# Optimization experiments

Measured on AMD Instinct MI355X. Metric: run time of the kernel, lower is better.

## Reference

```python
import jax, jax.numpy as jnp
import numpy as np

B, T, D, E, I = 8, 8192, 128, 8, 16
EPS = 1e-5


def setup_inputs() -> dict:
    key = jax.random.key(0)
    ks = jax.random.split(key, 6)
    return {
        "x": jax.random.normal(ks[0], (B, T, D), dtype=jnp.float32),
        "ln_g": jnp.ones((D,), dtype=jnp.float32),
        "ln_b": jnp.zeros((D,), dtype=jnp.float32),
        "gate_w": jax.random.normal(ks[1], (D, E), dtype=jnp.float32) * (1.0 / np.sqrt(D)),
        "gate_b": jnp.zeros((E,), dtype=jnp.float32),
        "w1": jax.random.normal(ks[2], (E, D, I), dtype=jnp.float32),
        "w2": jax.random.normal(ks[3], (E, I, D), dtype=jnp.float32),
    }


def reference(x, ln_g, ln_b, gate_w, gate_b, w1, w2):
    # LayerNorm (torch default eps=1e-5)
    mu = jnp.mean(x, axis=-1, keepdims=True)
    var = jnp.mean(jnp.square(x - mu), axis=-1, keepdims=True)
    x_norm = (x - mu) * jax.lax.rsqrt(var + EPS) * ln_g + ln_b

    # Dense gating + softmax routing
    gating_logits = x_norm @ gate_w + gate_b          # [B,T,E]
    routing_weights = jax.nn.softmax(gating_logits, axis=-1)

    # All-expert FFN: small batched GEMMs (torch F.gelu default = exact erf)
    y = jax.nn.gelu(jnp.einsum('btc,eci->btei', x_norm, w1), approximate=False)
    moe_experts_out = jnp.einsum('btei,eic->btec', y, w2)  # [B,T,E,D]
    moe_agg = jnp.einsum('btec,bte->btc', moe_experts_out, routing_weights)

    return (x + moe_agg, gating_logits, moe_experts_out)
```

## Files before the change

kernel.cpp:

```cpp
#include <hip/hip_runtime.h>
#include <math.h>

#define O1_OFF 8388608
#define O2_OFF 8912896

typedef __attribute__((ext_vector_type(8))) short short8;
typedef __attribute__((ext_vector_type(4))) float f32x4;

static __device__ __forceinline__ unsigned short f2bf(float f) {
    unsigned u = __builtin_bit_cast(unsigned, f);
    u = (u + 0x7fffu + ((u >> 16) & 1u)) >> 16;
    return (unsigned short)u;
}

static __device__ __forceinline__ int swz(int row, int chunk) {
    return row * 256 + ((chunk ^ (row & 7)) << 4);
}

static __device__ __forceinline__ int tswz(int row, int col) {
    int chunk = (col >> 3) ^ ((row >> 1) & 6);
    return row * 256 + (chunk << 4) + ((col & 7) << 1);
}

static __device__ __forceinline__ void bar_lds() {
    asm volatile("s_waitcnt lgkmcnt(0)" ::: "memory");
    __builtin_amdgcn_s_barrier();
    asm volatile("" ::: "memory");
}

static __device__ __forceinline__ void fence_lds() {
    asm volatile("s_waitcnt lgkmcnt(0)" ::: "memory");
}

__global__ __launch_bounds__(256, 2) void moe_fused(
    const float* __restrict__ x, const float* __restrict__ ln_g,
    const float* __restrict__ ln_b, const float* __restrict__ gate_w,
    const float* __restrict__ gate_b, const float* __restrict__ w1,
    const float* __restrict__ w2, float* __restrict__ out)
{
    __shared__ __align__(16) char smem[65536];
    char* pXY = smem;
    char* pW  = smem + 16384;
    char* pTR = smem + 49152;

    const int t = threadIdx.x;
    const int l = t & 63;
    const int w = t >> 6;
    const int tok0 = blockIdx.x * 64;

    const int colq = (t & 31) * 4;
    const int rsub = t >> 5;

    const int rb = w * 16;
    const int col = l & 15;
    const int ak = l >> 4;
    const int arow = rb + col;

    float4 xv[8];
    {
        const float* xb = x + (size_t)tok0 * 128;
        #pragma unroll
        for (int s = 0; s < 8; ++s)
            xv[s] = *(const float4*)(xb + s * 1024 + t * 4);
    }
    float4 g4 = *(const float4*)(ln_g + colq);
    float4 b4 = *(const float4*)(ln_b + colq);

    const int e2 = t >> 5;
    unsigned pk[4][8];
    {
        #pragma unroll
        for (int cc = 0; cc < 4; ++cc)
            #pragma unroll
            for (int q = 0; q < 8; ++q) pk[cc][q] = 0u;
        const float* w2b = w2 + e2 * 2048 + colq;
        #pragma unroll
        for (int i = 0; i < 16; ++i) {
            float4 q4 = *(const float4*)(w2b + i * 128);
            unsigned sh = (i & 1) * 16;
            pk[0][i >> 1] |= (unsigned)f2bf(q4.x) << sh;
            pk[1][i >> 1] |= (unsigned)f2bf(q4.y) << sh;
            pk[2][i >> 1] |= (unsigned)f2bf(q4.z) << sh;
            pk[3][i >> 1] |= (unsigned)f2bf(q4.w) << sh;
        }
    }

    {
        const int p = t & 127, ch = t >> 7;
        const float* w1b = w1 + (p >> 4) * 2048 + (p & 15);
        #pragma unroll
        for (int cc = 0; cc < 8; ++cc) {
            short8 v;
            #pragma unroll
            for (int j = 0; j < 8; ++j)
                v[j] = (short)f2bf(w1b[(ch * 64 + cc * 8 + j) * 16]);
            *(short8*)(pW + swz(p, ch * 8 + cc)) = v;
        }
    }

    short8 gfr[4];
    float gb;
    {
        #pragma unroll
        for (int ks = 0; ks < 4; ++ks)
            #pragma unroll
            for (int j = 0; j < 8; ++j) {
                float v = (col < 8) ? gate_w[(32 * ks + 8 * ak + j) * 8 + col] : 0.0f;
                gfr[ks][j] = (short)f2bf(v);
            }
        gb = (col < 8) ? gate_b[col] : 0.0f;
    }

    #pragma unroll
    for (int s = 0; s < 8; ++s) {
        float4 v = xv[s];
        float sm = v.x + v.y + v.z + v.w;
        float sq = v.x*v.x + v.y*v.y + v.z*v.z + v.w*v.w;
        #pragma unroll
        for (int m = 1; m < 32; m <<= 1) {
            sm += __shfl_xor(sm, m, 64);
            sq += __shfl_xor(sq, m, 64);
        }
        float mu = sm * (1.0f / 128.0f);
        float var = sq * (1.0f / 128.0f) - mu * mu;
        float rs = rsqrtf(var + 1e-5f);
        float n0 = (v.x - mu) * rs * g4.x + b4.x;
        float n1 = (v.y - mu) * rs * g4.y + b4.y;
        float n2 = (v.z - mu) * rs * g4.z + b4.z;
        float n3 = (v.w - mu) * rs * g4.w + b4.w;
        unsigned lo = (unsigned)f2bf(n0) | ((unsigned)f2bf(n1) << 16);
        unsigned hi = (unsigned)f2bf(n2) | ((unsigned)f2bf(n3) << 16);
        unsigned long long dvv = (unsigned long long)lo | ((unsigned long long)hi << 32);
        int row = s * 8 + rsub;
        *(unsigned long long*)(pXY + swz(row, colq >> 3) + (colq & 7) * 2) = dvv;
    }

    bar_lds();

    const f32x4 zero4 = {0.f, 0.f, 0.f, 0.f};
    const short8 zfrag = {0, 0, 0, 0, 0, 0, 0, 0};

    short8 afr[4];
    #pragma unroll
    for (int ks = 0; ks < 4; ++ks)
        afr[ks] = *(const short8*)(pXY + swz(arow, ks * 4 + ak));

    f32x4 accg = zero4;
    #pragma unroll
    for (int ks = 0; ks < 4; ++ks)
        accg = __builtin_amdgcn_mfma_f32_16x16x32_bf16(afr[ks], gfr[ks], accg, 0, 0, 0);

    float p_own[4];
    {
        float lg[4];
        #pragma unroll
        for (int r = 0; r < 4; ++r) lg[r] = accg[r] + gb;
        if (col < 8) {
            #pragma unroll
            for (int r = 0; r < 4; ++r)
                out[O1_OFF + (size_t)(tok0 + rb + ak * 4 + r) * 8 + col] = lg[r];
        }
        #pragma unroll
        for (int r = 0; r < 4; ++r) {
            float mx = lg[r];
            mx = fmaxf(mx, __shfl_xor(mx, 1, 64));
            mx = fmaxf(mx, __shfl_xor(mx, 2, 64));
            mx = fmaxf(mx, __shfl_xor(mx, 4, 64));
            float ex = __expf(lg[r] - mx);
            float smv = ex;
            smv += __shfl_xor(smv, 1, 64);
            smv += __shfl_xor(smv, 2, 64);
            smv += __shfl_xor(smv, 4, 64);
            p_own[r] = ex / smv;
        }
    }

    f32x4 accb[8];
    #pragma unroll
    for (int nt = 0; nt < 8; ++nt) accb[nt] = zero4;
    #pragma unroll
    for (int ks = 0; ks < 4; ++ks)
        #pragma unroll
        for (int nt = 0; nt < 8; ++nt) {
            short8 bfr = *(const short8*)(pW + swz(nt * 16 + col, ks * 4 + ak));
            accb[nt] = __builtin_amdgcn_mfma_f32_16x16x32_bf16(afr[ks], bfr, accb[nt], 0, 0, 0);
        }

    #pragma unroll
    for (int nt = 0; nt < 8; ++nt) {
        int chunkb = nt * 2 + (col >> 3);
        int off = (col & 7) * 2;
        #pragma unroll
        for (int r = 0; r < 4; ++r) {
            float s = accb[nt][r];
            float yv = 0.5f * s * (1.0f + erff(s * 0.70710678118654752f));
            *(unsigned short*)(pXY + swz(rb + ak * 4 + r, chunkb) + off) = f2bf(yv);
        }
    }

    bar_lds();

    #pragma unroll
    for (int cc = 0; cc < 4; ++cc) {
        int c = colq + cc;
        int rc = e2 * 128 + c;
        int a = (c >> 2) & 3;
        *(uint4*)(pW + (((rc * 2 + 0) ^ a) << 4)) =
            make_uint4(pk[cc][0], pk[cc][1], pk[cc][2], pk[cc][3]);
        *(uint4*)(pW + (((rc * 2 + 1) ^ a) << 4)) =
            make_uint4(pk[cc][4], pk[cc][5], pk[cc][6], pk[cc][7]);
    }

    bar_lds();

    f32x4 agg[8];
    #pragma unroll
    for (int nt = 0; nt < 8; ++nt) agg[nt] = zero4;

    #pragma unroll
    for (int e = 0; e < 8; ++e) {
        float rwe[4];
        #pragma unroll
        for (int r = 0; r < 4; ++r)
            rwe[r] = __shfl(p_own[r], (l & 48) + e, 64);
        short8 alo = *(const short8*)(pXY + swz(arow, 2 * e + (ak & 1)));
        short8 af = (ak < 2) ? alo : zfrag;
        f32x4 ot[8];
        #pragma unroll
        for (int nt = 0; nt < 8; ++nt) {
            int c = nt * 16 + col;
            int rc = e * 128 + c;
            int a = (c >> 2) & 3;
            short8 blo = *(const short8*)(pW + (((rc * 2 + (ak & 1)) ^ a) << 4));
            short8 bf = (ak < 2) ? blo : zfrag;
            ot[nt] = __builtin_amdgcn_mfma_f32_16x16x32_bf16(af, bf, zero4, 0, 0, 0);
            #pragma unroll
            for (int r = 0; r < 4; ++r)
                agg[nt][r] += rwe[r] * ot[nt][r];
        }
        #pragma unroll
        for (int nt = 0; nt < 8; ++nt)
            #pragma unroll
            for (int r = 0; r < 4; ++r)
                *(unsigned short*)(pTR + tswz(rb + ak * 4 + r, nt * 16 + col)) = f2bf(ot[nt][r]);
        fence_lds();
        #pragma unroll
        for (int i2 = 0; i2 < 8; ++i2) {
            int row = rb + i2 * 2 + (l >> 5);
            int c0 = (l & 31) * 4;
            unsigned long long raw = *(const unsigned long long*)(pTR + tswz(row, c0));
            unsigned lo = (unsigned)raw, hi = (unsigned)(raw >> 32);
            f32x4 v;
            v[0] = __builtin_bit_cast(float, lo << 16);
            v[1] = __builtin_bit_cast(float, lo & 0xffff0000u);
            v[2] = __builtin_bit_cast(float, hi << 16);
            v[3] = __builtin_bit_cast(float, hi & 0xffff0000u);
            *(f32x4*)(out + O2_OFF + (size_t)(tok0 + row) * 1024 + e * 128 + c0) = v;
        }
        asm volatile("" ::: "memory");
    }

    bar_lds();

    #pragma unroll
    for (int nt = 0; nt < 8; ++nt) {
        int c = nt * 16 + col;
        #pragma unroll
        for (int r = 0; r < 4; ++r) {
            int row = rb + ak * 4 + r;
            *(float*)(pW + row * 512 + ((c << 2) ^ ((row & 4) << 2))) = agg[nt][r];
        }
    }

    bar_lds();

    #pragma unroll
    for (int s = 0; s < 8; ++s) {
        int row = s * 8 + rsub;
        f32x4 a4 = *(const f32x4*)(pW + row * 512 + ((colq << 2) ^ ((row & 4) << 2)));
        float4 o;
        o.x = xv[s].x + a4[0];
        o.y = xv[s].y + a4[1];
        o.z = xv[s].z + a4[2];
        o.w = xv[s].w + a4[3];
        *(float4*)(out + (size_t)(tok0 + row) * 128 + colq) = o;
    }
}

extern "C" void kernel_launch(void* const* d_in, const int* in_sizes, int n_in,
                              void* d_out, int out_size, void* d_ws, size_t ws_size,
                              hipStream_t stream) {
    const float* x      = (const float*)d_in[0];
    const float* ln_g   = (const float*)d_in[1];
    const float* ln_b   = (const float*)d_in[2];
    const float* gate_w = (const float*)d_in[3];
    const float* gate_b = (const float*)d_in[4];
    const float* w1     = (const float*)d_in[5];
    const float* w2     = (const float*)d_in[6];
    float* out = (float*)d_out;
    (void)in_sizes; (void)n_in; (void)out_size; (void)d_ws; (void)ws_size;
    moe_fused<<<dim3(1024), dim3(256), 0, stream>>>(x, ln_g, ln_b, gate_w, gate_b, w1, w2, out);
}
```

Baseline: 84.03 us.

## Transpose MFMA operands to store expert outputs directly, dropping the LDS transpose

The MFMA operand order is swapped so each lane holds four consecutive output columns for a single token. That lets the fp32 expert outputs go straight to global memory with nontemporal vector stores, instead of being rounded to bf16 and transposed through LDS. Routing weights are passed through a small LDS buffer rather than shuffles. The residual add is rebuilt by staging x in LDS. With the LDS footprint reduced, launch bounds now ask for three blocks per CU. The trade-off is that each token's global writes become 64-byte segments scattered across rows, which is less contiguous than the earlier full-row stores.

```diff
diff --git a/kernel.cpp b/kernel.cpp
--- a/kernel.cpp
+++ b/kernel.cpp
@@ -17,31 +17,22 @@
     return row * 256 + ((chunk ^ (row & 7)) << 4);
 }
 
-static __device__ __forceinline__ int tswz(int row, int col) {
-    int chunk = (col >> 3) ^ ((row >> 1) & 6);
-    return row * 256 + (chunk << 4) + ((col & 7) << 1);
-}
-
 static __device__ __forceinline__ void bar_lds() {
     asm volatile("s_waitcnt lgkmcnt(0)" ::: "memory");
     __builtin_amdgcn_s_barrier();
     asm volatile("" ::: "memory");
 }
 
-static __device__ __forceinline__ void fence_lds() {
-    asm volatile("s_waitcnt lgkmcnt(0)" ::: "memory");
-}
-
-__global__ __launch_bounds__(256, 2) void moe_fused(
+__global__ __launch_bounds__(256, 3) void moe_fused(
     const float* __restrict__ x, const float* __restrict__ ln_g,
     const float* __restrict__ ln_b, const float* __restrict__ gate_w,
     const float* __restrict__ gate_b, const float* __restrict__ w1,
     const float* __restrict__ w2, float* __restrict__ out)
 {
-    __shared__ __align__(16) char smem[65536];
+    __shared__ __align__(16) char smem[51200];
     char* pXY = smem;
     char* pW  = smem + 16384;
-    char* pTR = smem + 49152;
+    float* pRW = (float*)(smem + 49152);
 
     const int t = threadIdx.x;
     const int l = t & 63;
@@ -52,9 +43,8 @@
     const int rsub = t >> 5;
 
     const int rb = w * 16;
-    const int col = l & 15;
+    const int tl = l & 15;
     const int ak = l >> 4;
-    const int arow = rb + col;
 
     float4 xv[8];
     {
@@ -99,16 +89,16 @@
     }
 
     short8 gfr[4];
-    float gb;
+    float4 gb4;
     {
         #pragma unroll
         for (int ks = 0; ks < 4; ++ks)
             #pragma unroll
             for (int j = 0; j < 8; ++j) {
-                float v = (col < 8) ? gate_w[(32 * ks + 8 * ak + j) * 8 + col] : 0.0f;
+                float v = (tl < 8) ? gate_w[(32 * ks + 8 * ak + j) * 8 + tl] : 0.0f;
                 gfr[ks][j] = (short)f2bf(v);
             }
-        gb = (col < 8) ? gate_b[col] : 0.0f;
+        gb4 = *(const float4*)(gate_b + (ak & 1) * 4);
     }
 
     #pragma unroll
@@ -143,35 +133,33 @@
     short8 afr[4];
     #pragma unroll
     for (int ks = 0; ks < 4; ++ks)
-        afr[ks] = *(const short8*)(pXY + swz(arow, ks * 4 + ak));
+        afr[ks] = *(const short8*)(pXY + swz(rb + tl, ks * 4 + ak));
 
     f32x4 accg = zero4;
     #pragma unroll
     for (int ks = 0; ks < 4; ++ks)
-        accg = __builtin_amdgcn_mfma_f32_16x16x32_bf16(afr[ks], gfr[ks], accg, 0, 0, 0);
-
-    float p_own[4];
-    {
-        float lg[4];
-        #pragma unroll
-        for (int r = 0; r < 4; ++r) lg[r] = accg[r] + gb;
-        if (col < 8) {
-            #pragma unroll
-            for (int r = 0; r < 4; ++r)
-                out[O1_OFF + (size_t)(tok0 + rb + ak * 4 + r) * 8 + col] = lg[r];
-        }
-        #pragma unroll
-        for (int r = 0; r < 4; ++r) {
-            float mx = lg[r];
-            mx = fmaxf(mx, __shfl_xor(mx, 1, 64));
-            mx = fmaxf(mx, __shfl_xor(mx, 2, 64));
-            mx = fmaxf(mx, __shfl_xor(mx, 4, 64));
-            float ex = __expf(lg[r] - mx);
-            float smv = ex;
-            smv += __shfl_xor(smv, 1, 64);
-            smv += __shfl_xor(smv, 2, 64);
-            smv += __shfl_xor(smv, 4, 64);
-            p_own[r] = ex / smv;
+        accg = __builtin_amdgcn_mfma_f32_16x16x32_bf16(gfr[ks], afr[ks], accg, 0, 0, 0);
+
+    const size_t trow = (size_t)(tok0 + rb + tl);
+    {
+        float lg0 = accg[0] + gb4.x;
+        float lg1 = accg[1] + gb4.y;
+        float lg2 = accg[2] + gb4.z;
+        float lg3 = accg[3] + gb4.w;
+        if (ak < 2) {
+            f32x4 lgv = {lg0, lg1, lg2, lg3};
+            __builtin_nontemporal_store(lgv, (f32x4*)(out + O1_OFF + trow * 8 + ak * 4));
+        }
+        float mx = fmaxf(fmaxf(lg0, lg1), fmaxf(lg2, lg3));
+        mx = fmaxf(mx, __shfl_xor(mx, 16, 64));
+        float ex0 = __expf(lg0 - mx), ex1 = __expf(lg1 - mx);
+        float ex2 = __expf(lg2 - mx), ex3 = __expf(lg3 - mx);
+        float sm = ex0 + ex1 + ex2 + ex3;
+        sm += __shfl_xor(sm, 16, 64);
+        float inv = 1.0f / sm;
+        if (ak < 2) {
+            f32x4 pv = {ex0 * inv, ex1 * inv, ex2 * inv, ex3 * inv};
+            *(f32x4*)(pRW + (rb + tl) * 8 + ak * 4) = pv;
         }
     }
 
@@ -182,20 +170,21 @@
     for (int ks = 0; ks < 4; ++ks)
         #pragma unroll
         for (int nt = 0; nt < 8; ++nt) {
-            short8 bfr = *(const short8*)(pW + swz(nt * 16 + col, ks * 4 + ak));
-            accb[nt] = __builtin_amdgcn_mfma_f32_16x16x32_bf16(afr[ks], bfr, accb[nt], 0, 0, 0);
+            short8 wfr = *(const short8*)(pW + swz(nt * 16 + tl, ks * 4 + ak));
+            accb[nt] = __builtin_amdgcn_mfma_f32_16x16x32_bf16(wfr, afr[ks], accb[nt], 0, 0, 0);
         }
 
     #pragma unroll
     for (int nt = 0; nt < 8; ++nt) {
-        int chunkb = nt * 2 + (col >> 3);
-        int off = (col & 7) * 2;
-        #pragma unroll
-        for (int r = 0; r < 4; ++r) {
-            float s = accb[nt][r];
-            float yv = 0.5f * s * (1.0f + erff(s * 0.70710678118654752f));
-            *(unsigned short*)(pXY + swz(rb + ak * 4 + r, chunkb) + off) = f2bf(yv);
-        }
+        float y0 = accb[nt][0], y1 = accb[nt][1], y2 = accb[nt][2], y3 = accb[nt][3];
+        y0 = 0.5f * y0 * (1.0f + erff(y0 * 0.70710678118654752f));
+        y1 = 0.5f * y1 * (1.0f + erff(y1 * 0.70710678118654752f));
+        y2 = 0.5f * y2 * (1.0f + erff(y2 * 0.70710678118654752f));
+        y3 = 0.5f * y3 * (1.0f + erff(y3 * 0.70710678118654752f));
+        unsigned lo = (unsigned)f2bf(y0) | ((unsigned)f2bf(y1) << 16);
+        unsigned hi = (unsigned)f2bf(y2) | ((unsigned)f2bf(y3) << 16);
+        unsigned long long dv = (unsigned long long)lo | ((unsigned long long)hi << 32);
+        *(unsigned long long*)(pXY + swz(rb + tl, nt * 2 + (ak >> 1)) + (ak & 1) * 8) = dv;
     }
 
     bar_lds();
@@ -213,62 +202,30 @@
 
     bar_lds();
 
+    f32x4 rwa = *(const f32x4*)(pRW + (rb + tl) * 8);
+    f32x4 rwb = *(const f32x4*)(pRW + (rb + tl) * 8 + 4);
+
     f32x4 agg[8];
     #pragma unroll
     for (int nt = 0; nt < 8; ++nt) agg[nt] = zero4;
 
+    float* o2b = out + O2_OFF + trow * 1024 + ak * 4;
     #pragma unroll
     for (int e = 0; e < 8; ++e) {
-        float rwe[4];
-        #pragma unroll
-        for (int r = 0; r < 4; ++r)
-            rwe[r] = __shfl(p_own[r], (l & 48) + e, 64);
-        short8 alo = *(const short8*)(pXY + swz(arow, 2 * e + (ak & 1)));
-        short8 af = (ak < 2) ? alo : zfrag;
-        f32x4 ot[8];
+        float rwe = (e < 4) ? rwa[e] : rwb[e - 4];
+        short8 ylo = *(const short8*)(pXY + swz(rb + tl, 2 * e + (ak & 1)));
+        short8 yf = (ak < 2) ? ylo : zfrag;
         #pragma unroll
         for (int nt = 0; nt < 8; ++nt) {
-            int c = nt * 16 + col;
-            int rc = e * 128 + c;
+            int c = nt * 16 + tl;
             int a = (c >> 2) & 3;
-            short8 blo = *(const short8*)(pW + (((rc * 2 + (ak & 1)) ^ a) << 4));
+            short8 blo = *(const short8*)(pW + e * 4096 + (((c * 2 + (ak & 1)) ^ a) << 4));
             short8 bf = (ak < 2) ? blo : zfrag;
-            ot[nt] = __builtin_amdgcn_mfma_f32_16x16x32_bf16(af, bf, zero4, 0, 0, 0);
+            f32x4 ot = __builtin_amdgcn_mfma_f32_16x16x32_bf16(bf, yf, zero4, 0, 0, 0);
+            __builtin_nontemporal_store(ot, (f32x4*)(o2b + e * 128 + nt * 16));
             #pragma unroll
             for (int r = 0; r < 4; ++r)
-                agg[nt][r] += rwe[r] * ot[nt][r];
-        }
-        #pragma unroll
-        for (int nt = 0; nt < 8; ++nt)
-            #pragma unroll
-            for (int r = 0; r < 4; ++r)
-                *(unsigned short*)(pTR + tswz(rb + ak * 4 + r, nt * 16 + col)) = f2bf(ot[nt][r]);
-        fence_lds();
-        #pragma unroll
-        for (int i2 = 0; i2 < 8; ++i2) {
-            int row = rb + i2 * 2 + (l >> 5);
-            int c0 = (l & 31) * 4;
-            unsigned long long raw = *(const unsigned long long*)(pTR + tswz(row, c0));
-            unsigned lo = (unsigned)raw, hi = (unsigned)(raw >> 32);
-            f32x4 v;
-            v[0] = __builtin_bit_cast(float, lo << 16);
-            v[1] = __builtin_bit_cast(float, lo & 0xffff0000u);
-            v[2] = __builtin_bit_cast(float, hi << 16);
-            v[3] = __builtin_bit_cast(float, hi & 0xffff0000u);
-            *(f32x4*)(out + O2_OFF + (size_t)(tok0 + row) * 1024 + e * 128 + c0) = v;
-        }
-        asm volatile("" ::: "memory");
-    }
-
-    bar_lds();
-
-    #pragma unroll
-    for (int nt = 0; nt < 8; ++nt) {
-        int c = nt * 16 + col;
-        #pragma unroll
-        for (int r = 0; r < 4; ++r) {
-            int row = rb + ak * 4 + r;
-            *(float*)(pW + row * 512 + ((c << 2) ^ ((row & 4) << 2))) = agg[nt][r];
+                agg[nt][r] += rwe * ot[r];
         }
     }
 
@@ -277,13 +234,19 @@
     #pragma unroll
     for (int s = 0; s < 8; ++s) {
         int row = s * 8 + rsub;
-        f32x4 a4 = *(const f32x4*)(pW + row * 512 + ((colq << 2) ^ ((row & 4) << 2)));
-        float4 o;
-        o.x = xv[s].x + a4[0];
-        o.y = xv[s].y + a4[1];
-        o.z = xv[s].z + a4[2];
-        o.w = xv[s].w + a4[3];
-        *(float4*)(out + (size_t)(tok0 + row) * 128 + colq) = o;
+        *(float4*)(pW + row * 512 + (((t & 31) ^ (row & 7)) << 4)) = xv[s];
+    }
+
+    bar_lds();
+
+    float* o0b = out + trow * 128 + ak * 4;
+    const int row0 = rb + tl;
+    #pragma unroll
+    for (int nt = 0; nt < 8; ++nt) {
+        int ch = nt * 4 + ak;
+        f32x4 xr = *(const f32x4*)(pW + row0 * 512 + ((ch ^ (row0 & 7)) << 4));
+        f32x4 o = xr + agg[nt];
+        __builtin_nontemporal_store(o, (f32x4*)(o0b + nt * 16));
     }
 }
 
```

Result: slower. 125.8 us (+49.7%).
